# Performance work log

Hardware: AMD Instinct MI355X
Metric: run time of the kernel (lower is better)

The kernel has to match this reference:

```python
import jax, jax.numpy as jnp
import numpy as np

N_NODES = 100000
N_EDGES = 3200000
N_GRAPHS = 256
F_IN, HID, OUT = 8, 64, 9


def gcn_conv(x, src, dst, W, b, n_nodes):
    """PyG GCNConv: x' = D^{-1/2}(A+I)D^{-1/2} (x W) + b, self-loops added."""
    h = x @ W  # [N, H] dense transform first (as in PyG)
    loop = jnp.arange(n_nodes, dtype=src.dtype)
    s = jnp.concatenate([src, loop])  # source of each message
    d = jnp.concatenate([dst, loop])  # destination (aggregation index)
    deg = jax.ops.segment_sum(jnp.ones_like(d, dtype=h.dtype), d, num_segments=n_nodes)
    dinv = jnp.where(deg > 0, jax.lax.rsqrt(deg), 0.0)
    norm = dinv[s] * dinv[d]  # [E+N]
    msg = h[s] * norm[:, None]  # gather + scale
    out = jax.ops.segment_sum(msg, d, num_segments=n_nodes)  # scatter-add
    return out + b


def setup_inputs() -> dict:
    key = jax.random.key(0)
    ks = jax.random.split(key, 20)

    def lin(k, fi, fo):
        bound = 1.0 / np.sqrt(fi)
        k1, k2 = jax.random.split(k)
        W = jax.random.uniform(k1, (fi, fo), jnp.float32, -bound, bound)
        b = jax.random.uniform(k2, (fo,), jnp.float32, -bound, bound)
        return W, b

    x = jax.random.normal(ks[0], (N_NODES, F_IN), jnp.float32)
    edge_index = jax.random.randint(ks[1], (2, N_EDGES), 0, N_NODES, jnp.int32)
    batch = jnp.sort(jax.random.randint(ks[2], (N_NODES,), 0, N_GRAPHS, jnp.int32))

    W1, b1 = lin(ks[3], F_IN, HID)
    W2, b2 = lin(ks[4], HID, HID)
    W3, b3 = lin(ks[5], HID, HID)
    Wg, bg = lin(ks[6], HID, HID)
    Wh1, bh1 = lin(ks[7], HID, HID // 2)
    Wh2, bh2 = lin(ks[8], HID // 2, 1)
    Wm1, bm1 = lin(ks[9], HID, HID)
    Wm2, bm2 = lin(ks[10], HID, OUT)
    Wp1, bp1 = lin(ks[11], HID, HID // 2)
    Wp2, bp2 = lin(ks[12], HID // 2, 1)

    return dict(x=x, edge_index=edge_index, batch=batch,
                W1=W1, b1=b1, W2=W2, b2=b2, W3=W3, b3=b3, Wg=Wg, bg=bg,
                Wh1=Wh1, bh1=bh1, Wh2=Wh2, bh2=bh2,
                Wm1=Wm1, bm1=bm1, Wm2=Wm2, bm2=bm2,
                Wp1=Wp1, bp1=bp1, Wp2=Wp2, bp2=bp2)


def reference(x, edge_index, batch,
              W1, b1, W2, b2, W3, b3, Wg, bg,
              Wh1, bh1, Wh2, bh2, Wm1, bm1, Wm2, bm2, Wp1, bp1, Wp2, bp2):
    src, dst = edge_index[0], edge_index[1]
    n = x.shape[0]

    h = jax.nn.relu(gcn_conv(x, src, dst, W1, b1, n))
    h = jax.nn.relu(gcn_conv(h, src, dst, W2, b2, n))
    h = gcn_conv(h, src, dst, W3, b3, n)

    # global_mean_pool over graphs in the batch
    sums = jax.ops.segment_sum(h, batch, num_segments=N_GRAPHS)
    cnts = jax.ops.segment_sum(jnp.ones((n,), h.dtype), batch, num_segments=N_GRAPHS)
    x_global = sums / jnp.maximum(cnts, 1.0)[:, None]
    x_global = jax.nn.relu(x_global @ Wg + bg)

    heuristic = jax.nn.relu(x_global @ Wh1 + bh1) @ Wh2 + bh2  # [B, 1]
    move_logits = jax.nn.relu(h @ Wm1 + bm1) @ Wm2 + bm2       # [N, 9]
    block_priority = jax.nn.relu(h @ Wp1 + bp1) @ Wp2 + bp2    # [N, 1]
    return heuristic, move_logits, block_priority
```

## Files before the change

kernel.cpp:

```cpp
#include <hip/hip_runtime.h>
#include <hip/hip_fp16.h>

#define N_NODES 100000
#define N_EDGES 3200000
#define N_GRAPHS 256
#define HID 64

#define BSHIFT 7
#define NPB 128
#define NBUCK 782
#define PCHUNK 8192
#define NPBLK 391
#define SCAP 5120

__global__ __launch_bounds__(256) void k_hist(
        const int* __restrict__ dst, int* __restrict__ hist) {
    __shared__ int h[NBUCK];
    int t = threadIdx.x;
    for (int j = t; j < NBUCK; j += 256) h[j] = 0;
    __syncthreads();
    int base = blockIdx.x * PCHUNK;
    int end = min(base + PCHUNK, N_EDGES);
    for (int i = base + t; i < end; i += 256)
        atomicAdd(&h[dst[i] >> BSHIFT], 1);
    __syncthreads();
    for (int j = t; j < NBUCK; j += 256) hist[j * NPBLK + blockIdx.x] = h[j];
}

__global__ __launch_bounds__(512) void k_scan_rows(
        int* __restrict__ hist, int* __restrict__ btotal) {
    __shared__ int s[512];
    int b = blockIdx.x, t = threadIdx.x;
    int v = (t < NPBLK) ? hist[b * NPBLK + t] : 0;
    s[t] = v;
    __syncthreads();
    for (int off = 1; off < 512; off <<= 1) {
        int add = (t >= off) ? s[t - off] : 0;
        __syncthreads();
        s[t] += add;
        __syncthreads();
    }
    if (t < NPBLK) hist[b * NPBLK + t] = s[t] - v;
    if (t == 511) btotal[b] = s[511];
}

__global__ __launch_bounds__(1024) void k_scan_base(
        const int* __restrict__ btotal, int* __restrict__ bbase,
        int* __restrict__ rowp_last) {
    __shared__ int s[1024];
    int t = threadIdx.x;
    int v = (t < NBUCK) ? btotal[t] : 0;
    s[t] = v;
    __syncthreads();
    for (int off = 1; off < 1024; off <<= 1) {
        int add = (t >= off) ? s[t - off] : 0;
        __syncthreads();
        s[t] += add;
        __syncthreads();
    }
    if (t < NBUCK) bbase[t] = s[t] - v;
    if (t == NBUCK - 1) rowp_last[0] = s[t];
}

__global__ __launch_bounds__(256) void k_scatter(
        const int* __restrict__ src, const int* __restrict__ dst,
        const int* __restrict__ hist, const int* __restrict__ bbase,
        unsigned* __restrict__ pairs) {
    __shared__ int cur[NBUCK];
    int t = threadIdx.x;
    for (int j = t; j < NBUCK; j += 256)
        cur[j] = bbase[j] + hist[j * NPBLK + blockIdx.x];
    __syncthreads();
    int base = blockIdx.x * PCHUNK;
    int end = min(base + PCHUNK, N_EDGES);
    for (int i = base + t; i < end; i += 256) {
        int d = dst[i], s = src[i];
        int b = d >> BSHIFT;
        int pos = atomicAdd(&cur[b], 1);
        pairs[pos] = (unsigned)s | ((unsigned)(d & (NPB - 1)) << 24);
    }
}

__global__ __launch_bounds__(256) void k_sort(
        const unsigned* __restrict__ pairs, const int* __restrict__ btotal,
        const int* __restrict__ bbase, int* __restrict__ esrc,
        int* __restrict__ rowp, float* __restrict__ dinv) {
    __shared__ int lcnt[NPB];
    __shared__ int lscan[NPB];
    __shared__ int lcur[NPB];
    __shared__ int lout[SCAP];
    int b = blockIdx.x, t = threadIdx.x;
    int nb = min(btotal[b], SCAP);
    int base = bbase[b];
    if (t < NPB) lcnt[t] = 0;
    __syncthreads();
    for (int i = t; i < nb; i += 256) atomicAdd(&lcnt[pairs[base + i] >> 24], 1);
    __syncthreads();
    if (t < NPB) lscan[t] = lcnt[t];
    __syncthreads();
    for (int off = 1; off < NPB; off <<= 1) {
        int add = (t < NPB && t >= off) ? lscan[t - off] : 0;
        __syncthreads();
        if (t < NPB) lscan[t] += add;
        __syncthreads();
    }
    if (t < NPB) lcur[t] = lscan[t] - lcnt[t];
    __syncthreads();
    for (int i = t; i < nb; i += 256) {
        unsigned u = pairs[base + i];
        int p = atomicAdd(&lcur[u >> 24], 1);
        lout[p] = (int)(u & 0x00FFFFFFu);
    }
    __syncthreads();
    for (int i = t; i < nb; i += 256) esrc[base + i] = lout[i];
    int node = b * NPB + t;
    if (t < NPB && node < N_NODES) {
        rowp[node] = base + lscan[t] - lcnt[t];
        dinv[node] = rsqrtf((float)lcnt[t] + 1.0f);
    }
}

__global__ __launch_bounds__(256) void k_fold(
        const float* __restrict__ W3, const float* __restrict__ b3,
        const float* __restrict__ Wm1, const float* __restrict__ bm1,
        const float* __restrict__ Wp1, const float* __restrict__ bp1,
        const float* __restrict__ Wg, const float* __restrict__ bg,
        float* __restrict__ Wpack, float* __restrict__ bpack,
        float* __restrict__ Wcg, float* __restrict__ bcg) {
    int tid = blockIdx.x * 256 + threadIdx.x;
    if (tid < 6144) {
        int k = tid / 96, c = tid % 96;
        float s = 0.f;
        if (c < 64) {
#pragma unroll 16
            for (int j = 0; j < 64; ++j) s += W3[k * 64 + j] * Wm1[j * 64 + c];
        } else {
            int cc = c - 64;
#pragma unroll 16
            for (int j = 0; j < 64; ++j) s += W3[k * 64 + j] * Wp1[j * 32 + cc];
        }
        Wpack[tid] = s;
    } else if (tid < 10240) {
        int t2 = tid - 6144;
        int k = t2 / 64, c = t2 % 64;
        float s = 0.f;
#pragma unroll 16
        for (int j = 0; j < 64; ++j) s += W3[k * 64 + j] * Wg[j * 64 + c];
        Wcg[t2] = s;
    } else if (tid < 10336) {
        int c = tid - 10240;
        float s;
        if (c < 64) {
            s = bm1[c];
            for (int j = 0; j < 64; ++j) s += b3[j] * Wm1[j * 64 + c];
        } else {
            int cc = c - 64;
            s = bp1[cc];
            for (int j = 0; j < 64; ++j) s += b3[j] * Wp1[j * 32 + cc];
        }
        bpack[c] = s;
    } else if (tid < 10400) {
        int c = tid - 10336;
        float s = bg[c];
        for (int j = 0; j < 64; ++j) s += b3[j] * Wg[j * 64 + c];
        bcg[c] = s;
    }
}

__global__ __launch_bounds__(256) void k_agg8t(
        const float* __restrict__ x, const float* __restrict__ dinv,
        const int* __restrict__ rp, const int* __restrict__ esrc,
        const float* __restrict__ W1, const float* __restrict__ b1,
        __half* __restrict__ Bout) {
    int wid = (blockIdx.x * 256 + threadIdx.x) >> 6;
    int lane = threadIdx.x & 63;
    if (wid >= N_NODES) return;
    int beg = rp[wid], end = rp[wid + 1];
    float4 lo = {0.f, 0.f, 0.f, 0.f}, hi = {0.f, 0.f, 0.f, 0.f};
    for (int e = beg + lane; e < end; e += 64) {
        int s = esrc[e];
        float dv = dinv[s];
        const float4* r = (const float4*)(x + (size_t)s * 8);
        float4 a = r[0], b = r[1];
        lo.x += dv * a.x; lo.y += dv * a.y; lo.z += dv * a.z; lo.w += dv * a.w;
        hi.x += dv * b.x; hi.y += dv * b.y; hi.z += dv * b.z; hi.w += dv * b.w;
    }
#pragma unroll
    for (int off = 32; off; off >>= 1) {
        lo.x += __shfl_xor(lo.x, off); lo.y += __shfl_xor(lo.y, off);
        lo.z += __shfl_xor(lo.z, off); lo.w += __shfl_xor(lo.w, off);
        hi.x += __shfl_xor(hi.x, off); hi.y += __shfl_xor(hi.y, off);
        hi.z += __shfl_xor(hi.z, off); hi.w += __shfl_xor(hi.w, off);
    }
    float dvw = dinv[wid];
    const float4* xr = (const float4*)(x + (size_t)wid * 8);
    float4 xa = xr[0], xb = xr[1];
    float y[8];
    y[0] = dvw * (lo.x + dvw * xa.x); y[1] = dvw * (lo.y + dvw * xa.y);
    y[2] = dvw * (lo.z + dvw * xa.z); y[3] = dvw * (lo.w + dvw * xa.w);
    y[4] = dvw * (hi.x + dvw * xb.x); y[5] = dvw * (hi.y + dvw * xb.y);
    y[6] = dvw * (hi.z + dvw * xb.z); y[7] = dvw * (hi.w + dvw * xb.w);
    float acc = b1[lane];
#pragma unroll
    for (int k = 0; k < 8; ++k) acc += y[k] * W1[k * 64 + lane];
    Bout[(size_t)wid * 64 + lane] = __float2half_rn(fmaxf(acc, 0.f) * dvw);
}

__global__ __launch_bounds__(256) void k_agg64h(
        const __half* __restrict__ B, float* __restrict__ Y,
        const float* __restrict__ dinv, const int* __restrict__ rp,
        const int* __restrict__ esrc) {
    int wid = (blockIdx.x * 256 + threadIdx.x) >> 6;
    int lane = threadIdx.x & 63;
    if (wid >= N_NODES) return;
    int beg = rp[wid], end = rp[wid + 1];
    int g = lane >> 3;
    int fl = (lane & 7) << 3;
    float a0[8], a1[8];
#pragma unroll
    for (int i = 0; i < 8; ++i) { a0[i] = 0.f; a1[i] = 0.f; }
    int e = beg + g;
    for (; e + 8 < end; e += 16) {
        int s0 = esrc[e];
        int s1 = esrc[e + 8];
        uint4 v0 = *(const uint4*)(B + (size_t)s0 * 64 + fl);
        uint4 v1 = *(const uint4*)(B + (size_t)s1 * 64 + fl);
        const __half2* h0 = (const __half2*)&v0;
        const __half2* h1 = (const __half2*)&v1;
#pragma unroll
        for (int i = 0; i < 4; ++i) {
            float2 f0 = __half22float2(h0[i]);
            float2 f1 = __half22float2(h1[i]);
            a0[2 * i] += f0.x; a0[2 * i + 1] += f0.y;
            a1[2 * i] += f1.x; a1[2 * i + 1] += f1.y;
        }
    }
    if (e < end) {
        int s0 = esrc[e];
        uint4 v0 = *(const uint4*)(B + (size_t)s0 * 64 + fl);
        const __half2* h0 = (const __half2*)&v0;
#pragma unroll
        for (int i = 0; i < 4; ++i) {
            float2 f0 = __half22float2(h0[i]);
            a0[2 * i] += f0.x; a0[2 * i + 1] += f0.y;
        }
    }
#pragma unroll
    for (int i = 0; i < 8; ++i) a0[i] += a1[i];
#pragma unroll
    for (int off = 8; off <= 32; off <<= 1) {
#pragma unroll
        for (int i = 0; i < 8; ++i) a0[i] += __shfl_xor(a0[i], off);
    }
    if (lane < 8) {
        uint4 sv = *(const uint4*)(B + (size_t)wid * 64 + fl);
        const __half2* sh = (const __half2*)&sv;
        float dv = dinv[wid];
        float r[8];
#pragma unroll
        for (int i = 0; i < 4; ++i) {
            float2 fs = __half22float2(sh[i]);
            r[2 * i]     = dv * (a0[2 * i] + fs.x);
            r[2 * i + 1] = dv * (a0[2 * i + 1] + fs.y);
        }
        float4 w0 = {r[0], r[1], r[2], r[3]};
        float4 w1 = {r[4], r[5], r[6], r[7]};
        float* yo = Y + (size_t)wid * 64 + fl;
        *(float4*)(yo) = w0;
        *(float4*)(yo + 4) = w1;
    }
}

template <int NCOL, int RELU, int SCALE, int PHEAD, int OUTH>
__global__ __launch_bounds__(NCOL * 4) void k_gemm(
        const float* __restrict__ A, const float* __restrict__ W,
        const float* __restrict__ bias, const float* __restrict__ dinv,
        float* __restrict__ out32, __half* __restrict__ out16,
        const float* __restrict__ Wp2, const float* __restrict__ bp2,
        float* __restrict__ out_p,
        const float* __restrict__ Wm2, const float* __restrict__ bm2,
        float* __restrict__ out_m) {
    __shared__ float Al[128 * 64];
    __shared__ float Wl[64 * NCOL];
    __shared__ float pbuf[PHEAD ? 128 * 8 : 4];
    __shared__ float wm2l[PHEAD ? 64 * 9 : 4];
    __shared__ float bm2l[PHEAD ? 9 : 1];
    const int NTHR = NCOL * 4;
    int tid = threadIdx.x;
    int base = blockIdx.x * 128;

    for (int idx = tid; idx < 128 * 16; idx += NTHR) {
        int r = idx >> 4, c4 = idx & 15;
        float4 v = {0.f, 0.f, 0.f, 0.f};
        if (base + r < N_NODES)
            v = *(const float4*)(A + (size_t)(base + r) * 64 + c4 * 4);
        *(float4*)(Al + r * 64 + c4 * 4) = v;
    }
    for (int idx = tid; idx < 64 * (NCOL / 4); idx += NTHR) {
        int r = idx / (NCOL / 4), c4 = idx % (NCOL / 4);
        *(float4*)(Wl + r * NCOL + c4 * 4) = *(const float4*)(W + r * NCOL + c4 * 4);
    }
    if (PHEAD) {
        for (int i = tid; i < 576; i += NTHR) wm2l[i] = Wm2[i];
        if (tid < 9) bm2l[tid] = bm2[tid];
    }
    __syncthreads();

    int tc = tid % (NCOL / 4);
    int tr = tid / (NCOL / 4);

    float acc[8][4];
#pragma unroll
    for (int i = 0; i < 8; ++i)
#pragma unroll
        for (int c = 0; c < 4; ++c) acc[i][c] = 0.f;

    for (int kb = 0; kb < 16; ++kb) {
        float w0[4], w1[4], w2[4], w3[4];
        {
            const float* wp = Wl + (kb * 4) * NCOL + tc * 4;
            float4 a = *(const float4*)(wp);
            float4 b = *(const float4*)(wp + NCOL);
            float4 c = *(const float4*)(wp + 2 * NCOL);
            float4 d = *(const float4*)(wp + 3 * NCOL);
            w0[0] = a.x; w0[1] = a.y; w0[2] = a.z; w0[3] = a.w;
            w1[0] = b.x; w1[1] = b.y; w1[2] = b.z; w1[3] = b.w;
            w2[0] = c.x; w2[1] = c.y; w2[2] = c.z; w2[3] = c.w;
            w3[0] = d.x; w3[1] = d.y; w3[2] = d.z; w3[3] = d.w;
        }
#pragma unroll
        for (int i = 0; i < 8; ++i) {
            float4 af = *(const float4*)(Al + (tr * 8 + i) * 64 + kb * 4);
#pragma unroll
            for (int c = 0; c < 4; ++c)
                acc[i][c] += af.x * w0[c] + af.y * w1[c] + af.z * w2[c] + af.w * w3[c];
        }
    }

    if (PHEAD) __syncthreads();

    float4 bv = *(const float4*)(bias + tc * 4);
    float wp2l[4] = {0.f, 0.f, 0.f, 0.f};
    if (PHEAD && tc >= 16) {
        float4 wv = *(const float4*)(Wp2 + (tc - 16) * 4);
        wp2l[0] = wv.x; wp2l[1] = wv.y; wp2l[2] = wv.z; wp2l[3] = wv.w;
    }
#pragma unroll
    for (int i = 0; i < 8; ++i) {
        int lr = tr * 8 + i;
        int r = base + lr;
        bool ok = r < N_NODES;
        float o0 = acc[i][0] + bv.x, o1 = acc[i][1] + bv.y;
        float o2 = acc[i][2] + bv.z, o3 = acc[i][3] + bv.w;
        if (RELU) {
            o0 = fmaxf(o0, 0.f); o1 = fmaxf(o1, 0.f);
            o2 = fmaxf(o2, 0.f); o3 = fmaxf(o3, 0.f);
        }
        if (SCALE) {
            float dv = ok ? dinv[r] : 0.f;
            o0 *= dv; o1 *= dv; o2 *= dv; o3 *= dv;
        }
        if (PHEAD) {
            if (tc >= 16) {
                pbuf[lr * 8 + (tc - 16)] =
                    o0 * wp2l[0] + o1 * wp2l[1] + o2 * wp2l[2] + o3 * wp2l[3];
            } else {
                float4 st = {o0, o1, o2, o3};
                *(float4*)(Al + lr * 64 + tc * 4) = st;
            }
        } else if (ok) {
            if (OUTH) {
                __half2 h01 = __halves2half2(__float2half_rn(o0), __float2half_rn(o1));
                __half2 h23 = __halves2half2(__float2half_rn(o2), __float2half_rn(o3));
                __half2* dst = (__half2*)(out16 + (size_t)r * 64 + tc * 4);
                dst[0] = h01; dst[1] = h23;
            } else {
                float4 st = {o0, o1, o2, o3};
                *(float4*)(out32 + (size_t)r * 64 + tc * 4) = st;
            }
        }
    }
    if (PHEAD) {
        __syncthreads();
        for (int o = tid; o < 128 * 9; o += NTHR) {
            int rr = o / 9, j = o - rr * 9;
            int node = base + rr;
            if (node < N_NODES) {
                float s = bm2l[j];
#pragma unroll 16
                for (int k = 0; k < 64; ++k) s += Al[rr * 64 + k] * wm2l[k * 9 + j];
                out_m[(size_t)node * 9 + j] = s;
            }
        }
        if (tid < 128) {
            int r = base + tid;
            if (r < N_NODES) {
                float s = 0.f;
#pragma unroll
                for (int j = 0; j < 8; ++j) s += pbuf[tid * 8 + j];
                out_p[r] = s + bp2[0];
            }
        }
    }
}

__global__ __launch_bounds__(256) void k_graphhead(
        const float* __restrict__ A, const int* __restrict__ batch,
        const float* __restrict__ Wcg, const float* __restrict__ bcg,
        const float* __restrict__ Wh1, const float* __restrict__ bh1,
        const float* __restrict__ Wh2, const float* __restrict__ bh2,
        float* __restrict__ out_h) {
    __shared__ float l[256];
    __shared__ float xgp[64];
    __shared__ float xg[64];
    int gph = blockIdx.x;
    int t = threadIdx.x;
    int lo = 0, hi = N_NODES;
    int target = (t & 1) ? gph + 1 : gph;
    while (lo < hi) {
        int mid = (lo + hi) >> 1;
        if (batch[mid] < target) lo = mid + 1; else hi = mid;
    }
    __shared__ int bounds[2];
    if (t < 2) bounds[t] = lo;
    __syncthreads();
    int beg = bounds[0], end = bounds[1];

    int lane = t & 63, grp = t >> 6;
    float acc = 0.f;
    for (int r = beg + grp; r < end; r += 4) acc += A[(size_t)r * 64 + lane];
    l[t] = acc;
    __syncthreads();
    if (t < 64) {
        float s = l[t] + l[t + 64] + l[t + 128] + l[t + 192];
        xgp[t] = s / fmaxf((float)(end - beg), 1.f);
    }
    __syncthreads();
    {
        int c = t & 63, q = t >> 6;
        float p = 0.f;
#pragma unroll
        for (int k = 0; k < 16; ++k)
            p += xgp[q * 16 + k] * Wcg[(q * 16 + k) * 64 + c];
        l[t] = p;
        __syncthreads();
        if (t < 64)
            xg[t] = fmaxf(l[t] + l[t + 64] + l[t + 128] + l[t + 192] + bcg[t], 0.f);
    }
    __syncthreads();
    if (t < 32) {
        float hj = bh1[t];
#pragma unroll 16
        for (int k = 0; k < 64; ++k) hj += xg[k] * Wh1[k * 32 + t];
        float q = fmaxf(hj, 0.f) * Wh2[t];
#pragma unroll
        for (int off = 16; off; off >>= 1) q += __shfl_xor(q, off);
        if (t == 0) out_h[gph] = q + bh2[0];
    }
}


extern "C" void kernel_launch(void* const* d_in, const int* in_sizes, int n_in,
                              void* d_out, int out_size, void* d_ws, size_t ws_size,
                              hipStream_t stream) {
    const float* x    = (const float*)d_in[0];
    const int*   ei   = (const int*)d_in[1];
    const int*   batch= (const int*)d_in[2];
    const float* W1   = (const float*)d_in[3];
    const float* b1   = (const float*)d_in[4];
    const float* W2   = (const float*)d_in[5];
    const float* b2   = (const float*)d_in[6];
    const float* W3   = (const float*)d_in[7];
    const float* b3   = (const float*)d_in[8];
    const float* Wg   = (const float*)d_in[9];
    const float* bg   = (const float*)d_in[10];
    const float* Wh1  = (const float*)d_in[11];
    const float* bh1  = (const float*)d_in[12];
    const float* Wh2  = (const float*)d_in[13];
    const float* bh2  = (const float*)d_in[14];
    const float* Wm1  = (const float*)d_in[15];
    const float* bm1  = (const float*)d_in[16];
    const float* Wm2  = (const float*)d_in[17];
    const float* bm2  = (const float*)d_in[18];
    const float* Wp1  = (const float*)d_in[19];
    const float* bp1  = (const float*)d_in[20];
    const float* Wp2  = (const float*)d_in[21];
    const float* bp2  = (const float*)d_in[22];

    const int* e_src = ei;
    const int* e_dst = ei + N_EDGES;

    char* ws = (char*)d_ws;
    size_t off = 0;
    auto alloc = [&](size_t bytes) {
        void* p = ws + off;
        off += (bytes + 255) & ~(size_t)255;
        return p;
    };
    float* bufA   = (float*)alloc(N_NODES * 64 * sizeof(float));
    float* bufB   = (float*)alloc(N_NODES * 64 * sizeof(float));
    float* dinv   = (float*)alloc(N_NODES * sizeof(float));
    int*   rowp   = (int*)  alloc((N_NODES + 1) * sizeof(int));
    int*   esrc   = (int*)  alloc(N_EDGES * sizeof(int));
    int*   hist   = (int*)  alloc((size_t)NBUCK * NPBLK * sizeof(int));
    int*   btotal = (int*)  alloc(NBUCK * sizeof(int));
    int*   bbase  = (int*)  alloc(NBUCK * sizeof(int));
    float* Wpack  = (float*)alloc(64 * 96 * sizeof(float));
    float* bpack  = (float*)alloc(96 * sizeof(float));
    float* Wcg    = (float*)alloc(64 * 64 * sizeof(float));
    float* bcg    = (float*)alloc(64 * sizeof(float));
    unsigned* pairs = (unsigned*)bufA;
    __half* B2h = (__half*)bufB;
    __half* B3h = (__half*)(bufB + 3200000);
    (void)ws_size; (void)n_in; (void)in_sizes; (void)out_size;

    float* out_h = (float*)d_out;
    float* out_m = (float*)d_out + 256;
    float* out_p = (float*)d_out + 256 + 900000;

    const int TB = 256;
    dim3 blkWave((N_NODES * 64 + TB - 1) / TB);
    const int NT = 782;

    k_hist<<<NPBLK, TB, 0, stream>>>(e_dst, hist);
    k_scan_rows<<<NBUCK, 512, 0, stream>>>(hist, btotal);
    k_scan_base<<<1, 1024, 0, stream>>>(btotal, bbase, rowp + N_NODES);
    k_scatter<<<NPBLK, TB, 0, stream>>>(e_src, e_dst, hist, bbase, pairs);
    k_sort<<<NBUCK, TB, 0, stream>>>(pairs, btotal, bbase, esrc, rowp, dinv);

    k_fold<<<41, TB, 0, stream>>>(W3, b3, Wm1, bm1, Wp1, bp1, Wg, bg,
                                  Wpack, bpack, Wcg, bcg);

    k_agg8t<<<blkWave, TB, 0, stream>>>(x, dinv, rowp, esrc, W1, b1, B2h);
    k_agg64h<<<blkWave, TB, 0, stream>>>(B2h, bufA, dinv, rowp, esrc);
    k_gemm<64, 1, 1, 0, 1><<<NT, 256, 0, stream>>>(
        bufA, W2, b2, dinv, nullptr, B3h,
        nullptr, nullptr, nullptr, nullptr, nullptr, nullptr);
    k_agg64h<<<blkWave, TB, 0, stream>>>(B3h, bufA, dinv, rowp, esrc);

    k_gemm<96, 1, 0, 1, 0><<<NT, 384, 0, stream>>>(
        bufA, Wpack, bpack, nullptr, nullptr, nullptr,
        Wp2, bp2, out_p, Wm2, bm2, out_m);

    k_graphhead<<<N_GRAPHS, TB, 0, stream>>>(bufA, batch, Wcg, bcg,
                                             Wh1, bh1, Wh2, bh2, out_h);
}
```

Baseline: 350.6 us.

## Shrink partition chunks, transpose histogram layout, prepack pre-scaled half features for layer one

```diff
diff --git a/kernel.cpp b/kernel.cpp
--- a/kernel.cpp
+++ b/kernel.cpp
@@ -9,8 +9,8 @@
 #define BSHIFT 7
 #define NPB 128
 #define NBUCK 782
-#define PCHUNK 8192
-#define NPBLK 391
+#define PCHUNK 2048
+#define NPBLK 1563
 #define SCAP 5120
 
 __global__ __launch_bounds__(256) void k_hist(
@@ -24,24 +24,37 @@
     for (int i = base + t; i < end; i += 256)
         atomicAdd(&h[dst[i] >> BSHIFT], 1);
     __syncthreads();
-    for (int j = t; j < NBUCK; j += 256) hist[j * NPBLK + blockIdx.x] = h[j];
-}
-
-__global__ __launch_bounds__(512) void k_scan_rows(
+    for (int j = t; j < NBUCK; j += 256)
+        hist[(size_t)blockIdx.x * NBUCK + j] = h[j];
+}
+
+__global__ __launch_bounds__(1024) void k_scan_rows(
         int* __restrict__ hist, int* __restrict__ btotal) {
-    __shared__ int s[512];
+    __shared__ int s[1024];
+    __shared__ int carry_s;
     int b = blockIdx.x, t = threadIdx.x;
-    int v = (t < NPBLK) ? hist[b * NPBLK + t] : 0;
-    s[t] = v;
-    __syncthreads();
-    for (int off = 1; off < 512; off <<= 1) {
-        int add = (t >= off) ? s[t - off] : 0;
-        __syncthreads();
-        s[t] += add;
-        __syncthreads();
-    }
-    if (t < NPBLK) hist[b * NPBLK + t] = s[t] - v;
-    if (t == 511) btotal[b] = s[511];
+    if (t == 0) carry_s = 0;
+    __syncthreads();
+    for (int base = 0; base < NPBLK; base += 1024) {
+        int idx = base + t;
+        int v = (idx < NPBLK) ? hist[(size_t)idx * NBUCK + b] : 0;
+        s[t] = v;
+        __syncthreads();
+        for (int off = 1; off < 1024; off <<= 1) {
+            int add = (t >= off) ? s[t - off] : 0;
+            __syncthreads();
+            s[t] += add;
+            __syncthreads();
+        }
+        int inc = s[t];
+        int total = s[1023];
+        int c = carry_s;
+        if (idx < NPBLK) hist[(size_t)idx * NBUCK + b] = c + inc - v;
+        __syncthreads();
+        if (t == 0) carry_s = c + total;
+        __syncthreads();
+    }
+    if (t == 0) btotal[b] = carry_s;
 }
 
 __global__ __launch_bounds__(1024) void k_scan_base(
@@ -69,7 +82,7 @@
     __shared__ int cur[NBUCK];
     int t = threadIdx.x;
     for (int j = t; j < NBUCK; j += 256)
-        cur[j] = bbase[j] + hist[j * NPBLK + blockIdx.x];
+        cur[j] = bbase[j] + hist[(size_t)blockIdx.x * NBUCK + j];
     __syncthreads();
     int base = blockIdx.x * PCHUNK;
     int end = min(base + PCHUNK, N_EDGES);
@@ -167,43 +180,67 @@
     }
 }
 
+__global__ __launch_bounds__(256) void k_prepack(
+        const float* __restrict__ x, const float* __restrict__ dinv,
+        __half* __restrict__ xsh) {
+    int n = blockIdx.x * 256 + threadIdx.x;
+    if (n >= N_NODES) return;
+    float dv = dinv[n];
+    const float4* xr = (const float4*)(x + (size_t)n * 8);
+    float4 a = xr[0], b = xr[1];
+    __half2 h0 = __halves2half2(__float2half_rn(a.x * dv), __float2half_rn(a.y * dv));
+    __half2 h1 = __halves2half2(__float2half_rn(a.z * dv), __float2half_rn(a.w * dv));
+    __half2 h2 = __halves2half2(__float2half_rn(b.x * dv), __float2half_rn(b.y * dv));
+    __half2 h3 = __halves2half2(__float2half_rn(b.z * dv), __float2half_rn(b.w * dv));
+    __half2* o = (__half2*)(xsh + (size_t)n * 8);
+    o[0] = h0; o[1] = h1; o[2] = h2; o[3] = h3;
+}
+
 __global__ __launch_bounds__(256) void k_agg8t(
-        const float* __restrict__ x, const float* __restrict__ dinv,
+        const __half* __restrict__ xsh, const float* __restrict__ dinv,
         const int* __restrict__ rp, const int* __restrict__ esrc,
         const float* __restrict__ W1, const float* __restrict__ b1,
         __half* __restrict__ Bout) {
-    int wid = (blockIdx.x * 256 + threadIdx.x) >> 6;
-    int lane = threadIdx.x & 63;
-    if (wid >= N_NODES) return;
-    int beg = rp[wid], end = rp[wid + 1];
-    float4 lo = {0.f, 0.f, 0.f, 0.f}, hi = {0.f, 0.f, 0.f, 0.f};
-    for (int e = beg + lane; e < end; e += 64) {
+    int gid = (blockIdx.x * 256 + threadIdx.x) >> 5;
+    int l = threadIdx.x & 31;
+    if (gid >= N_NODES) return;
+    int beg = rp[gid], end = rp[gid + 1];
+    float a[8];
+#pragma unroll
+    for (int i = 0; i < 8; ++i) a[i] = 0.f;
+    for (int e = beg + l; e < end; e += 32) {
         int s = esrc[e];
-        float dv = dinv[s];
-        const float4* r = (const float4*)(x + (size_t)s * 8);
-        float4 a = r[0], b = r[1];
-        lo.x += dv * a.x; lo.y += dv * a.y; lo.z += dv * a.z; lo.w += dv * a.w;
-        hi.x += dv * b.x; hi.y += dv * b.y; hi.z += dv * b.z; hi.w += dv * b.w;
-    }
-#pragma unroll
-    for (int off = 32; off; off >>= 1) {
-        lo.x += __shfl_xor(lo.x, off); lo.y += __shfl_xor(lo.y, off);
-        lo.z += __shfl_xor(lo.z, off); lo.w += __shfl_xor(lo.w, off);
-        hi.x += __shfl_xor(hi.x, off); hi.y += __shfl_xor(hi.y, off);
-        hi.z += __shfl_xor(hi.z, off); hi.w += __shfl_xor(hi.w, off);
-    }
-    float dvw = dinv[wid];
-    const float4* xr = (const float4*)(x + (size_t)wid * 8);
-    float4 xa = xr[0], xb = xr[1];
+        uint4 v = *(const uint4*)(xsh + (size_t)s * 8);
+        const __half2* h = (const __half2*)&v;
+#pragma unroll
+        for (int i = 0; i < 4; ++i) {
+            float2 f = __half22float2(h[i]);
+            a[2 * i] += f.x; a[2 * i + 1] += f.y;
+        }
+    }
+#pragma unroll
+    for (int off = 1; off < 32; off <<= 1) {
+#pragma unroll
+        for (int i = 0; i < 8; ++i) a[i] += __shfl_xor(a[i], off);
+    }
+    float dvw = dinv[gid];
+    uint4 sv = *(const uint4*)(xsh + (size_t)gid * 8);
+    const __half2* sh = (const __half2*)&sv;
     float y[8];
-    y[0] = dvw * (lo.x + dvw * xa.x); y[1] = dvw * (lo.y + dvw * xa.y);
-    y[2] = dvw * (lo.z + dvw * xa.z); y[3] = dvw * (lo.w + dvw * xa.w);
-    y[4] = dvw * (hi.x + dvw * xb.x); y[5] = dvw * (hi.y + dvw * xb.y);
-    y[6] = dvw * (hi.z + dvw * xb.z); y[7] = dvw * (hi.w + dvw * xb.w);
-    float acc = b1[lane];
-#pragma unroll
-    for (int k = 0; k < 8; ++k) acc += y[k] * W1[k * 64 + lane];
-    Bout[(size_t)wid * 64 + lane] = __float2half_rn(fmaxf(acc, 0.f) * dvw);
+#pragma unroll
+    for (int i = 0; i < 4; ++i) {
+        float2 fs = __half22float2(sh[i]);
+        y[2 * i]     = dvw * (a[2 * i] + fs.x);
+        y[2 * i + 1] = dvw * (a[2 * i + 1] + fs.y);
+    }
+    float acc0 = b1[l], acc1 = b1[l + 32];
+#pragma unroll
+    for (int k = 0; k < 8; ++k) {
+        acc0 += y[k] * W1[k * 64 + l];
+        acc1 += y[k] * W1[k * 64 + l + 32];
+    }
+    Bout[(size_t)gid * 64 + l]      = __float2half_rn(fmaxf(acc0, 0.f) * dvw);
+    Bout[(size_t)gid * 64 + l + 32] = __float2half_rn(fmaxf(acc1, 0.f) * dvw);
 }
 
 __global__ __launch_bounds__(256) void k_agg64h(
@@ -505,6 +542,7 @@
     int*   hist   = (int*)  alloc((size_t)NBUCK * NPBLK * sizeof(int));
     int*   btotal = (int*)  alloc(NBUCK * sizeof(int));
     int*   bbase  = (int*)  alloc(NBUCK * sizeof(int));
+    __half* xsh   = (__half*)alloc(N_NODES * 8 * sizeof(__half));
     float* Wpack  = (float*)alloc(64 * 96 * sizeof(float));
     float* bpack  = (float*)alloc(96 * sizeof(float));
     float* Wcg    = (float*)alloc(64 * 64 * sizeof(float));
@@ -520,10 +558,11 @@
 
     const int TB = 256;
     dim3 blkWave((N_NODES * 64 + TB - 1) / TB);
+    dim3 blkHalf((N_NODES * 32 + TB - 1) / TB);
     const int NT = 782;
 
     k_hist<<<NPBLK, TB, 0, stream>>>(e_dst, hist);
-    k_scan_rows<<<NBUCK, 512, 0, stream>>>(hist, btotal);
+    k_scan_rows<<<NBUCK, 1024, 0, stream>>>(hist, btotal);
     k_scan_base<<<1, 1024, 0, stream>>>(btotal, bbase, rowp + N_NODES);
     k_scatter<<<NPBLK, TB, 0, stream>>>(e_src, e_dst, hist, bbase, pairs);
     k_sort<<<NBUCK, TB, 0, stream>>>(pairs, btotal, bbase, esrc, rowp, dinv);
@@ -531,7 +570,8 @@
     k_fold<<<41, TB, 0, stream>>>(W3, b3, Wm1, bm1, Wp1, bp1, Wg, bg,
                                   Wpack, bpack, Wcg, bcg);
 
-    k_agg8t<<<blkWave, TB, 0, stream>>>(x, dinv, rowp, esrc, W1, b1, B2h);
+    k_prepack<<<(N_NODES + TB - 1) / TB, TB, 0, stream>>>(x, dinv, xsh);
+    k_agg8t<<<blkHalf, TB, 0, stream>>>(xsh, dinv, rowp, esrc, W1, b1, B2h);
     k_agg64h<<<blkWave, TB, 0, stream>>>(B2h, bufA, dinv, rowp, esrc);
     k_gemm<64, 1, 1, 0, 1><<<NT, 256, 0, stream>>>(
         bufA, W2, b2, dinv, nullptr, B3h,
```

Measured after the change: 350.8 us. Within noise of the previous version (+0.1%).
